# Kernel optimization log

Measured on AMD Instinct MI355X. Metric: run time of the kernel, lower is better.

The kernel has to match this reference:

```python
import math
import jax, jax.numpy as jnp
import numpy as np

N_HEAD = 16
ROPE_BASE = 10000.0


def _rope_tables(T, half, dtype):
    # build_sin_cos(seq_len, dim=head_dim//2): inv freq of length `half`
    pos = jnp.arange(T, dtype=jnp.float32)[:, None]                       # (T,1)
    inv = jnp.exp(jnp.arange(0, 2 * half, 2, dtype=jnp.float32) * (-math.log(ROPE_BASE) / (2 * half)))
    ang = pos * inv                                                        # (T, half)
    return jnp.sin(ang).astype(dtype), jnp.cos(ang).astype(dtype)


def _apply_rope(q, k, sin, cos):
    # q,k: (B,T,H,Dh); sin,cos: (T, Dh//2) -> broadcast over batch and heads
    half = q.shape[-1] // 2
    s = sin[None, :, None, :]
    c = cos[None, :, None, :]
    q1, q2 = q[..., :half], q[..., half:]
    k1, k2 = k[..., :half], k[..., half:]
    q = jnp.concatenate([q1 * c - q2 * s, q2 * c + q1 * s], axis=-1)
    k = jnp.concatenate([k1 * c - k2 * s, k2 * c + k1 * s], axis=-1)
    return q, k


def setup_inputs() -> dict:
    key = jax.random.key(0)
    k1, k2, k3 = jax.random.split(key, 3)
    B, T, C = 2, 2048, 2048
    x = jax.random.normal(k1, (B, T, C), dtype=jnp.float32)
    w_qkv = jax.random.normal(k2, (3 * C, C), dtype=jnp.float32) * (1.0 / math.sqrt(C))
    w_proj = jax.random.normal(k3, (C, C), dtype=jnp.float32) * (1.0 / math.sqrt(C))
    return {"x": x, "w_qkv": w_qkv, "w_proj": w_proj}


def reference(x, w_qkv, w_proj):
    B, T, C = x.shape
    H = N_HEAD
    Dh = C // H
    # fused QKV projection (Linear, no bias): (B,T,3C) -> (B,T,3,H,Dh)
    qkv = jnp.einsum('btc,oc->bto', x, w_qkv).reshape(B, T, 3, H, Dh)
    q, k, v = qkv[:, :, 0], qkv[:, :, 1], qkv[:, :, 2]          # (B,T,H,Dh)
    sin, cos = _rope_tables(T, Dh // 2, x.dtype)
    q, k = _apply_rope(q, k, sin, cos)
    # causal attention, scale 1/sqrt(Dh) (flash default softmax_scale=None)
    scale = 1.0 / math.sqrt(Dh)
    scores = jnp.einsum('bqhd,bkhd->bhqk', q, k) * scale        # (B,H,T,T)
    mask = jnp.tril(jnp.ones((T, T), dtype=bool))
    scores = jnp.where(mask[None, None], scores, jnp.finfo(scores.dtype).min)
    probs = jax.nn.softmax(scores, axis=-1)
    out = jnp.einsum('bhqk,bkhd->bqhd', probs, v)               # (B,T,H,Dh)
    # faithful to original: permute(0,2,1,3) then reshape_as(x)
    out = jnp.transpose(out, (0, 2, 1, 3)).reshape(B, T, C)
    return jnp.einsum('btc,oc->bto', out, w_proj)
```

## Files before the change

kernel.cpp:

```cpp
#include <hip/hip_runtime.h>
#include <hip/hip_bf16.h>

typedef __bf16 bf16_t;
typedef __bf16 bf16x8 __attribute__((ext_vector_type(8)));
typedef float f32x4 __attribute__((ext_vector_type(4)));

#define MFMA16(a, b, c) __builtin_amdgcn_mfma_f32_16x16x32_bf16(a, b, c, 0, 0, 0)

__device__ __forceinline__ void async_copy16(const void* g, void* l) {
  __builtin_amdgcn_global_load_lds(
      (const __attribute__((address_space(1))) void*)g,
      (__attribute__((address_space(3))) void*)l, 16, 0, 0);
}

__global__ void cast_f32_bf16(const float* __restrict__ in, bf16_t* __restrict__ out, int n8) {
  int stride = gridDim.x * blockDim.x;
  for (int i = blockIdx.x * blockDim.x + threadIdx.x; i < n8; i += stride) {
    const float* p = in + (size_t)i * 8;
    f32x4 a = *(const f32x4*)p;
    f32x4 b = *(const f32x4*)(p + 4);
    bf16x8 o;
    o[0] = (bf16_t)a[0]; o[1] = (bf16_t)a[1]; o[2] = (bf16_t)a[2]; o[3] = (bf16_t)a[3];
    o[4] = (bf16_t)b[0]; o[5] = (bf16_t)b[1]; o[6] = (bf16_t)b[2]; o[7] = (bf16_t)b[3];
    *(bf16x8*)(out + (size_t)i * 8) = o;
  }
}

template <int MODE>
__global__ __launch_bounds__(512, 2) void gemm256(
    const bf16_t* __restrict__ A, const bf16_t* __restrict__ Bw, float* __restrict__ C,
    bf16_t* __restrict__ qo, bf16_t* __restrict__ ko, bf16_t* __restrict__ vto,
    int M, int N, int K, int nby) {
  __shared__ __align__(16) char lds[98304];
  int tid = threadIdx.x;
  int w = tid >> 6, lane = tid & 63;
  int wm = w >> 1, wn = w & 1;
  int mr = lane & 15, kg = lane >> 4;

  int nwg = gridDim.x;
  int orig = blockIdx.x;
  int wgid = (orig & 7) * (nwg >> 3) + (orig >> 3);
  int by = wgid % nby, bx = wgid / nby;
  int row0 = by * 256, col0 = bx * 128;

  size_t aoff[4], boff[2];
#pragma unroll
  for (int it = 0; it < 4; ++it) {
    int c = tid + it * 512;
    int r = c >> 3;
    int chs = (c & 7) ^ (r & 7);
    aoff[it] = (size_t)(row0 + r) * K + chs * 8;
  }
#pragma unroll
  for (int it = 0; it < 2; ++it) {
    int c = tid + it * 512;
    int r = c >> 3;
    int chs = (c & 7) ^ (r & 7);
    boff[it] = (size_t)(col0 + r) * K + chs * 8;
  }

  auto stage = [&](int buf, int kt) {
    char* Ad = &lds[buf * 32768];
    char* Bd = &lds[65536 + buf * 16384];
#pragma unroll
    for (int it = 0; it < 4; ++it)
      async_copy16(A + aoff[it] + kt * 64, Ad + (tid + it * 512) * 16);
#pragma unroll
    for (int it = 0; it < 2; ++it)
      async_copy16(Bw + boff[it] + kt * 64, Bd + (tid + it * 512) * 16);
  };

  f32x4 zero = {0.f, 0.f, 0.f, 0.f};
  f32x4 acc[4][4];
#pragma unroll
  for (int mi = 0; mi < 4; ++mi)
#pragma unroll
    for (int ni = 0; ni < 4; ++ni) acc[mi][ni] = zero;

  int nt = K >> 6;
  stage(0, 0);
#pragma unroll 1
  for (int t = 0; t < nt; ++t) {
    int cur = t & 1;
    stage(cur ^ 1, (t + 1 < nt) ? (t + 1) : t);
    asm volatile("s_waitcnt vmcnt(6)" ::: "memory");
    __builtin_amdgcn_sched_barrier(0);
    __builtin_amdgcn_s_barrier();
    __builtin_amdgcn_sched_barrier(0);
    const char* Ab = &lds[cur * 32768];
    const char* Bb = &lds[65536 + cur * 16384];
    bf16x8 af[4][2];
#pragma unroll
    for (int mi = 0; mi < 4; ++mi) {
      int row = wm * 64 + mi * 16 + mr;
      const char* rb = Ab + row * 128;
      int sz = (row & 7) << 4;
      af[mi][0] = *(const bf16x8*)(rb + ((kg * 16) ^ sz));
      af[mi][1] = *(const bf16x8*)(rb + ((64 + kg * 16) ^ sz));
    }
#pragma unroll
    for (int ni = 0; ni < 4; ++ni) {
      int row = wn * 64 + ni * 16 + mr;
      const char* rb = Bb + row * 128;
      int sz = (row & 7) << 4;
      bf16x8 b0 = *(const bf16x8*)(rb + ((kg * 16) ^ sz));
      bf16x8 b1 = *(const bf16x8*)(rb + ((64 + kg * 16) ^ sz));
      __builtin_amdgcn_s_setprio(1);
#pragma unroll
      for (int mi = 0; mi < 4; ++mi) {
        acc[mi][ni] = MFMA16(af[mi][0], b0, acc[mi][ni]);
        acc[mi][ni] = MFMA16(af[mi][1], b1, acc[mi][ni]);
      }
      __builtin_amdgcn_s_setprio(0);
    }
    __builtin_amdgcn_sched_barrier(0);
    __builtin_amdgcn_s_barrier();
    __builtin_amdgcn_sched_barrier(0);
  }
  asm volatile("s_waitcnt vmcnt(0)" ::: "memory");
  __syncthreads();

  if (MODE == 0) {
#pragma unroll
    for (int mi = 0; mi < 4; ++mi)
#pragma unroll
      for (int ni = 0; ni < 4; ++ni)
#pragma unroll
        for (int jj = 0; jj < 4; ++jj) {
          int row = row0 + wm * 64 + mi * 16 + kg * 4 + jj;
          int col = col0 + wn * 64 + ni * 16 + mr;
          C[(size_t)row * N + col] = acc[mi][ni][jj];
        }
  } else {
    char* tb = &lds[0];
    int s = col0 >> 11, h = (col0 >> 7) & 15;
    int b = row0 >> 11, t0 = row0 & 2047;
    if (s < 2) {
#pragma unroll
      for (int mi = 0; mi < 4; ++mi)
#pragma unroll
        for (int ni = 0; ni < 4; ++ni)
#pragma unroll
          for (int jj = 0; jj < 4; ++jj) {
            int rloc = wm * 64 + mi * 16 + kg * 4 + jj;
            int cb = (wn * 64 + ni * 16 + mr) * 2;
            *(bf16_t*)(tb + rloc * 256 + (cb ^ ((rloc & 7) << 4))) = (bf16_t)acc[mi][ni][jj];
          }
      __syncthreads();
      int r = tid >> 1, hh = tid & 1;
      const char* rowb = tb + r * 256;
      int sz = (r & 7) << 4;
      int t = t0 + r;
      bf16_t* dst = (s == 0 ? qo : ko) + ((size_t)((b * 16 + h) * 2048 + t)) * 128 + hh * 64;
      float tf = (float)t;
      const float cinv = -0.20762050593046014f;
#pragma unroll
      for (int m = 0; m < 8; ++m) {
        bf16x8 va = *(const bf16x8*)(rowb + ((hh * 128 + m * 16) ^ sz));
        bf16x8 vb = *(const bf16x8*)(rowb + (((hh ^ 1) * 128 + m * 16) ^ sz));
        bf16x8 o;
#pragma unroll
        for (int e = 0; e < 8; ++e) {
          float ang = tf * exp2f((float)(m * 8 + e) * cinv);
          float sv = __sinf(ang), cv = __cosf(ang);
          float x1 = (float)va[e], x2 = (float)vb[e];
          o[e] = (bf16_t)((hh == 0) ? (x1 * cv - x2 * sv) : (x1 * cv + x2 * sv));
        }
        *(bf16x8*)(dst + m * 8) = o;
      }
    } else {
#pragma unroll
      for (int mi = 0; mi < 4; ++mi)
#pragma unroll
        for (int ni = 0; ni < 4; ++ni)
#pragma unroll
          for (int jj = 0; jj < 4; ++jj) {
            int rloc = wm * 64 + mi * 16 + kg * 4 + jj;
            int cloc = wn * 64 + ni * 16 + mr;
            *(bf16_t*)(tb + cloc * 512 + ((rloc * 2) ^ ((cloc & 7) << 4))) =
                (bf16_t)acc[mi][ni][jj];
          }
      __syncthreads();
      int d = tid >> 2, qt = tid & 3;
      const char* rowb = tb + d * 512;
      int sz = (d & 7) << 4;
      bf16_t* dst = vto + ((size_t)((b * 16 + h) * 128 + d)) * 2048 + t0 + qt * 64;
#pragma unroll
      for (int m2 = 0; m2 < 8; ++m2)
        *(bf16x8*)(dst + m2 * 8) = *(const bf16x8*)(rowb + ((qt * 128 + m2 * 16) ^ sz));
    }
  }
}

__global__ __launch_bounds__(256) void attn_kernel(
    const bf16_t* __restrict__ qg, const bf16_t* __restrict__ kgl,
    const bf16_t* __restrict__ vtg, bf16_t* __restrict__ og) {
  __shared__ __align__(16) bf16_t Ks[2][64 * 128];
  __shared__ __align__(16) bf16_t Vs[2][128 * 64];
  __shared__ __align__(16) bf16_t plds[4][1024];
  const int T = 2048;
  int tid = threadIdx.x;
  int w = tid >> 6, lane = tid & 63;
  int mr = lane & 15, kg = lane >> 4;
  int swz = (mr & 7) << 4;

  int L = blockIdx.y * 16 + blockIdx.x;
  int role = (L & 7) * 64 + (L >> 3);
  int bx = role & 15, bh = role >> 4;

  const bf16_t* Q = qg + (size_t)bh * T * 128;
  const bf16_t* K = kgl + (size_t)bh * T * 128;
  const bf16_t* Vt = vtg + (size_t)bh * 128 * T;

  int sb = tid * 16;
  int krl = sb >> 8;
  int kc = (sb & 255) ^ ((krl & 7) << 4);
  size_t ksrc = (size_t)krl * 128 + (kc >> 1);
  int vdl = sb >> 7;
  int vc = (sb & 127) ^ ((vdl & 7) << 4);
  size_t vsrc = (size_t)vdl * 2048 + (vc >> 1);

  auto stage = [&](int buf, int kb) {
#pragma unroll
    for (int it = 0; it < 4; ++it)
      async_copy16(K + (size_t)(kb + it * 16) * 128 + ksrc, &Ks[buf][it * 2048 + tid * 8]);
#pragma unroll
    for (int it = 0; it < 4; ++it)
      async_copy16(Vt + (size_t)it * 65536 + kb + vsrc, &Vs[buf][it * 2048 + tid * 8]);
  };

  const float cscale = 0.12751744f;
  f32x4 zero = {0.f, 0.f, 0.f, 0.f};
  bf16_t* P = &plds[w][0];
  int b = bh >> 4, h = bh & 15;

#pragma unroll 1
  for (int ph = 0; ph < 2; ++ph) {
    int qb = ph ? bx : (31 - bx);
    int qr0 = qb * 64 + w * 16;
    bf16x8 qf[4];
#pragma unroll
    for (int db = 0; db < 4; ++db)
      qf[db] = *(const bf16x8*)(Q + (size_t)(qr0 + mr) * 128 + db * 32 + kg * 8);

    f32x4 acc[8];
#pragma unroll
    for (int d2 = 0; d2 < 8; ++d2) acc[d2] = zero;
    float mrun[4] = {-1e30f, -1e30f, -1e30f, -1e30f};
    float lrun[4] = {0.f, 0.f, 0.f, 0.f};

    int nj = qb + 1;
    __syncthreads();
    stage(0, 0);
    int cur = 0;
#pragma unroll 1
    for (int j = 0; j < nj; ++j) {
      __syncthreads();
      if (j + 1 < nj) stage(cur ^ 1, (j + 1) * 64);
      const char* KsB = (const char*)&Ks[cur][0];
      const char* VsB = (const char*)&Vs[cur][0];
      int kb = j * 64;
      f32x4 s[4];
#pragma unroll
      for (int ntl = 0; ntl < 4; ++ntl) {
        s[ntl] = zero;
        int rowb = (ntl * 16 + mr) * 256;
#pragma unroll
        for (int db = 0; db < 4; ++db) {
          bf16x8 kf = *(const bf16x8*)(KsB + rowb + ((db * 64 + kg * 16) ^ swz));
          s[ntl] = MFMA16(qf[db], kf, s[ntl]);
        }
      }
      float pvv[4][4];
      float tmax[4] = {-3e38f, -3e38f, -3e38f, -3e38f};
      bool diag = (j == qb);
#pragma unroll
      for (int ntl = 0; ntl < 4; ++ntl)
#pragma unroll
        for (int jj = 0; jj < 4; ++jj) {
          float v = s[ntl][jj] * cscale;
          if (diag && (kb + ntl * 16 + mr) > (qr0 + kg * 4 + jj)) v = -1e30f;
          pvv[ntl][jj] = v;
          tmax[jj] = fmaxf(tmax[jj], v);
        }
#pragma unroll
      for (int m = 1; m < 16; m <<= 1)
#pragma unroll
        for (int jj = 0; jj < 4; ++jj)
          tmax[jj] = fmaxf(tmax[jj], __shfl_xor(tmax[jj], m, 64));
      bool ok = true;
#pragma unroll
      for (int jj = 0; jj < 4; ++jj) ok &= (tmax[jj] <= mrun[jj] + 8.0f);
      if (!__all(ok)) {
#pragma unroll
        for (int jj = 0; jj < 4; ++jj) {
          float mn = fmaxf(mrun[jj], tmax[jj]);
          float corr = __builtin_amdgcn_exp2f(mrun[jj] - mn);
          mrun[jj] = mn;
          lrun[jj] *= corr;
#pragma unroll
          for (int d2 = 0; d2 < 8; ++d2) acc[d2][jj] *= corr;
        }
      }
      float rs[4] = {0.f, 0.f, 0.f, 0.f};
#pragma unroll
      for (int ntl = 0; ntl < 4; ++ntl)
#pragma unroll
        for (int jj = 0; jj < 4; ++jj) {
          float p = __builtin_amdgcn_exp2f(pvv[ntl][jj] - mrun[jj]);
          pvv[ntl][jj] = p;
          rs[jj] += p;
        }
#pragma unroll
      for (int m = 1; m < 16; m <<= 1)
#pragma unroll
        for (int jj = 0; jj < 4; ++jj) rs[jj] += __shfl_xor(rs[jj], m, 64);
#pragma unroll
      for (int jj = 0; jj < 4; ++jj) lrun[jj] += rs[jj];
#pragma unroll
      for (int ntl = 0; ntl < 4; ++ntl)
#pragma unroll
        for (int jj = 0; jj < 4; ++jj) {
          int rr = kg * 4 + jj;
          int cbyte = (mr + ntl * 16) * 2;
          *(bf16_t*)((char*)P + rr * 128 + (cbyte ^ ((rr & 7) << 4))) = (bf16_t)pvv[ntl][jj];
        }
#pragma unroll
      for (int ks = 0; ks < 2; ++ks) {
        int cb = (ks * 32 + kg * 8) * 2;
        bf16x8 pa = *(const bf16x8*)((const char*)P + mr * 128 + (cb ^ ((mr & 7) << 4)));
#pragma unroll
        for (int d2 = 0; d2 < 8; ++d2) {
          bf16x8 vf = *(const bf16x8*)(VsB + (d2 * 16 + mr) * 128 + ((ks * 64 + kg * 16) ^ swz));
          acc[d2] = MFMA16(pa, vf, acc[d2]);
        }
      }
      cur ^= 1;
    }
#pragma unroll
    for (int jj = 0; jj < 4; ++jj) {
      float invl = 1.0f / lrun[jj];
      int t = qr0 + kg * 4 + jj;
      size_t row = (size_t)b * 2048 + h * 128 + (t >> 4);
      bf16_t* orow = og + row * 2048 + (t & 15) * 128;
#pragma unroll
      for (int d2 = 0; d2 < 8; ++d2)
        orow[d2 * 16 + mr] = (bf16_t)(acc[d2][jj] * invl);
    }
  }
}

extern "C" void kernel_launch(void* const* d_in, const int* in_sizes, int n_in,
                              void* d_out, int out_size, void* d_ws, size_t ws_size,
                              hipStream_t stream) {
  const float* x = (const float*)d_in[0];
  const float* wqkv = (const float*)d_in[1];
  const float* wproj = (const float*)d_in[2];
  float* out = (float*)d_out;
  char* ws = (char*)d_ws;

  const size_t OFF_WQKV = 16777216;
  const size_t OFF_Q = 41943040;
  const size_t OFF_K = 58720256;
  const size_t OFF_VT = 75497472;

  bf16_t* xb = (bf16_t*)(ws);
  bf16_t* wqkvb = (bf16_t*)(ws + OFF_WQKV);
  bf16_t* g_q = (bf16_t*)(ws + OFF_Q);
  bf16_t* g_k = (bf16_t*)(ws + OFF_K);
  bf16_t* g_vt = (bf16_t*)(ws + OFF_VT);
  bf16_t* g_att = (bf16_t*)(ws);
  bf16_t* wprojb = (bf16_t*)(ws + OFF_WQKV);

  cast_f32_bf16<<<2048, 256, 0, stream>>>(x, xb, 8388608 / 8);
  cast_f32_bf16<<<2048, 256, 0, stream>>>(wqkv, wqkvb, 12582912 / 8);
  gemm256<1><<<768, 512, 0, stream>>>(xb, wqkvb, nullptr, g_q, g_k, g_vt,
                                      4096, 6144, 2048, 16);
  cast_f32_bf16<<<2048, 256, 0, stream>>>(wproj, wprojb, 4194304 / 8);
  attn_kernel<<<dim3(16, 32), 256, 0, stream>>>(g_q, g_k, g_vt, g_att);
  gemm256<0><<<256, 512, 0, stream>>>(g_att, wprojb, out, nullptr, nullptr, nullptr,
                                      4096, 2048, 2048, 16);
}
```

Before: 286.1 us.

## Triple-buffer GEMM LDS stages and interleave async loads with MFMA groups

The bf16 GEMM moves from a 2-stage to a 3-stage LDS ring buffer, prefetching two K-tiles ahead with one barrier per iteration instead of two. All B fragments are now read from LDS up front. The next tile's global-to-LDS copies are split into three chunks issued between groups of MFMAs, so memory traffic overlaps compute. The cost is more LDS per block (144KB) and more live fragment registers, which may reduce occupancy or increase register pressure.

```diff
diff --git a/kernel.cpp b/kernel.cpp
--- a/kernel.cpp
+++ b/kernel.cpp
@@ -31,7 +31,7 @@
     const bf16_t* __restrict__ A, const bf16_t* __restrict__ Bw, float* __restrict__ C,
     bf16_t* __restrict__ qo, bf16_t* __restrict__ ko, bf16_t* __restrict__ vto,
     int M, int N, int K, int nby) {
-  __shared__ __align__(16) char lds[98304];
+  __shared__ __align__(16) char lds[147456];
   int tid = threadIdx.x;
   int w = tid >> 6, lane = tid & 63;
   int wm = w >> 1, wn = w & 1;
@@ -59,12 +59,14 @@
     boff[it] = (size_t)(col0 + r) * K + chs * 8;
   }
 
-  auto stage = [&](int buf, int kt) {
-    char* Ad = &lds[buf * 32768];
-    char* Bd = &lds[65536 + buf * 16384];
-#pragma unroll
-    for (int it = 0; it < 4; ++it)
+  auto stageA = [&](int buf, int kt, int half) {
+    char* Ad = &lds[buf * 49152];
+#pragma unroll
+    for (int it = half * 2; it < half * 2 + 2; ++it)
       async_copy16(A + aoff[it] + kt * 64, Ad + (tid + it * 512) * 16);
+  };
+  auto stageB = [&](int buf, int kt) {
+    char* Bd = &lds[buf * 49152 + 32768];
 #pragma unroll
     for (int it = 0; it < 2; ++it)
       async_copy16(Bw + boff[it] + kt * 64, Bd + (tid + it * 512) * 16);
@@ -78,18 +80,21 @@
     for (int ni = 0; ni < 4; ++ni) acc[mi][ni] = zero;
 
   int nt = K >> 6;
-  stage(0, 0);
+  stageA(0, 0, 0); stageA(0, 0, 1); stageB(0, 0);
+  stageA(1, 1, 0); stageA(1, 1, 1); stageB(1, 1);
+  asm volatile("s_waitcnt vmcnt(6)" ::: "memory");
+  __builtin_amdgcn_sched_barrier(0);
+  __builtin_amdgcn_s_barrier();
+  __builtin_amdgcn_sched_barrier(0);
+
 #pragma unroll 1
   for (int t = 0; t < nt; ++t) {
-    int cur = t & 1;
-    stage(cur ^ 1, (t + 1 < nt) ? (t + 1) : t);
-    asm volatile("s_waitcnt vmcnt(6)" ::: "memory");
-    __builtin_amdgcn_sched_barrier(0);
-    __builtin_amdgcn_s_barrier();
-    __builtin_amdgcn_sched_barrier(0);
-    const char* Ab = &lds[cur * 32768];
-    const char* Bb = &lds[65536 + cur * 16384];
-    bf16x8 af[4][2];
+    int cur = t % 3;
+    int nxt = (t + 2) % 3;
+    int kt2 = (t + 2 < nt) ? (t + 2) : t;
+    const char* Ab = &lds[cur * 49152];
+    const char* Bb = &lds[cur * 49152 + 32768];
+    bf16x8 af[4][2], bfr[4][2];
 #pragma unroll
     for (int mi = 0; mi < 4; ++mi) {
       int row = wm * 64 + mi * 16 + mr;
@@ -103,16 +108,36 @@
       int row = wn * 64 + ni * 16 + mr;
       const char* rb = Bb + row * 128;
       int sz = (row & 7) << 4;
-      bf16x8 b0 = *(const bf16x8*)(rb + ((kg * 16) ^ sz));
-      bf16x8 b1 = *(const bf16x8*)(rb + ((64 + kg * 16) ^ sz));
-      __builtin_amdgcn_s_setprio(1);
-#pragma unroll
-      for (int mi = 0; mi < 4; ++mi) {
-        acc[mi][ni] = MFMA16(af[mi][0], b0, acc[mi][ni]);
-        acc[mi][ni] = MFMA16(af[mi][1], b1, acc[mi][ni]);
-      }
-      __builtin_amdgcn_s_setprio(0);
-    }
+      bfr[ni][0] = *(const bf16x8*)(rb + ((kg * 16) ^ sz));
+      bfr[ni][1] = *(const bf16x8*)(rb + ((64 + kg * 16) ^ sz));
+    }
+    stageA(nxt, kt2, 0);
+    __builtin_amdgcn_s_setprio(1);
+#pragma unroll
+    for (int mi = 0; mi < 4; ++mi) {
+      acc[mi][0] = MFMA16(af[mi][0], bfr[0][0], acc[mi][0]);
+      acc[mi][0] = MFMA16(af[mi][1], bfr[0][1], acc[mi][0]);
+    }
+    __builtin_amdgcn_s_setprio(0);
+    stageA(nxt, kt2, 1);
+    __builtin_amdgcn_s_setprio(1);
+#pragma unroll
+    for (int mi = 0; mi < 4; ++mi) {
+      acc[mi][1] = MFMA16(af[mi][0], bfr[1][0], acc[mi][1]);
+      acc[mi][1] = MFMA16(af[mi][1], bfr[1][1], acc[mi][1]);
+    }
+    __builtin_amdgcn_s_setprio(0);
+    stageB(nxt, kt2);
+    __builtin_amdgcn_s_setprio(1);
+#pragma unroll
+    for (int mi = 0; mi < 4; ++mi) {
+      acc[mi][2] = MFMA16(af[mi][0], bfr[2][0], acc[mi][2]);
+      acc[mi][2] = MFMA16(af[mi][1], bfr[2][1], acc[mi][2]);
+      acc[mi][3] = MFMA16(af[mi][0], bfr[3][0], acc[mi][3]);
+      acc[mi][3] = MFMA16(af[mi][1], bfr[3][1], acc[mi][3]);
+    }
+    __builtin_amdgcn_s_setprio(0);
+    asm volatile("s_waitcnt vmcnt(6)" ::: "memory");
     __builtin_amdgcn_sched_barrier(0);
     __builtin_amdgcn_s_barrier();
     __builtin_amdgcn_sched_barrier(0);
```

New measurement: 277.7 us. 2.9% less time.
